# Performance work log

Hardware: AMD Instinct MI355X
Metric: run time of the kernel (lower is better)

Reference implementation:

```python
import jax, jax.numpy as jnp
import numpy as np

GROUPS = 8   # channels // group_size with group_size=8 for C=64
EPS = 1e-5


def group_norm_qc(x0, x1, gamma, beta):
    """LatticeGroupNorm: stats computed jointly over both cosets per (batch, group)."""
    B, C, H, W = x0.shape
    g = GROUPS
    xg = jnp.concatenate([x0.reshape(B, g, -1), x1.reshape(B, g, -1)], axis=-1)
    mean = xg.mean(axis=-1).reshape(B, g, 1, 1, 1)
    var = xg.var(axis=-1).reshape(B, g, 1, 1, 1)
    inv = jax.lax.rsqrt(var + EPS)
    ga = gamma[None, :, None, None]
    be = beta[None, :, None, None]

    def norm(x):
        xr = x.reshape(B, g, C // g, H, W)
        return ((xr - mean) * inv).reshape(B, C, H, W) * ga + be

    return norm(x0), norm(x1)


def qc_conv(x0, x1, w_center, w_corner, bias):
    """Quincunx LatticePad+LatticeConvolution with stencil
    [(0,0),(2,0),(0,2),(2,2),(1,1)], center (1,1).
    w_center: [O,I] tap (1,1) (same-coset 1x1).
    w_corner: [O,I,2,2] taps (0,0),(2,0),(0,2),(2,2) (cross-coset 2x2).
    Pad keeps output cosets the same size as inputs ('same' lattice conv)."""
    dn = ('NCHW', 'OIHW', 'NCHW')

    def c1(x):
        return jnp.einsum('oi,bihw->bohw', w_center, x)

    def c2(x, pad):
        return jax.lax.conv_general_dilated(x, w_corner, (1, 1), pad,
                                            dimension_numbers=dn)

    b = bias[None, :, None, None]
    # coset0 output gathers coset1 at (i-1+a, j-1+b) -> pad top/left
    out0 = c1(x0) + c2(x1, ((1, 0), (1, 0))) + b
    # coset1 output gathers coset0 at (i+a, j+b) -> pad bottom/right
    out1 = c1(x1) + c2(x0, ((0, 1), (0, 1))) + b
    return out0, out1


def setup_inputs() -> dict:
    key = jax.random.key(0)
    ks = jax.random.split(key, 10)
    B, C, H, W = 2, 64, 256, 256
    s = 0.05
    return {
        'x0': jax.random.normal(ks[0], (B, C, H, W), jnp.float32),
        'x1': jax.random.normal(ks[1], (B, C, H, W), jnp.float32),
        'g1': jnp.ones((C,), jnp.float32),
        'b1': jnp.zeros((C,), jnp.float32),
        'w1_center': jax.random.normal(ks[2], (C, C), jnp.float32) * s,
        'w1_corner': jax.random.normal(ks[3], (C, C, 2, 2), jnp.float32) * s,
        'bias1': jax.random.normal(ks[4], (C,), jnp.float32) * s,
        'g2': jnp.ones((C,), jnp.float32),
        'b2': jnp.zeros((C,), jnp.float32),
        'w2_center': jax.random.normal(ks[5], (C, C), jnp.float32) * s,
        'w2_corner': jax.random.normal(ks[6], (C, C, 2, 2), jnp.float32) * s,
        'bias2': jax.random.normal(ks[7], (C,), jnp.float32) * s,
        'w_skip': jax.random.normal(ks[8], (C, C), jnp.float32) * s,
        'bias_skip': jax.random.normal(ks[9], (C,), jnp.float32) * s,
        'g_skip': jnp.ones((C,), jnp.float32),
        'beta_skip': jnp.zeros((C,), jnp.float32),
    }


def reference(x0, x1, g1, b1, w1_center, w1_corner, bias1,
              g2, b2, w2_center, w2_corner, bias2,
              w_skip, bias_skip, g_skip, beta_skip):
    # conv path: GN -> ReLU -> pad+conv -> GN -> ReLU -> pad+conv
    h0, h1 = group_norm_qc(x0, x1, g1, b1)
    h0, h1 = jax.nn.relu(h0), jax.nn.relu(h1)
    h0, h1 = qc_conv(h0, h1, w1_center, w1_corner, bias1)
    h0, h1 = group_norm_qc(h0, h1, g2, b2)
    h0, h1 = jax.nn.relu(h0), jax.nn.relu(h1)
    h0, h1 = qc_conv(h0, h1, w2_center, w2_corner, bias2)
    # skip path: 1x1 lattice conv (stencil [(0,0)]) -> GN
    bsk = bias_skip[None, :, None, None]
    s0 = jnp.einsum('oi,bihw->bohw', w_skip, x0) + bsk
    s1 = jnp.einsum('oi,bihw->bohw', w_skip, x1) + bsk
    s0, s1 = group_norm_qc(s0, s1, g_skip, beta_skip)
    # residual add; stack the two cosets as leading axis for a single output
    return jnp.stack([h0 + s0, h1 + s1])
```

## Files before the change

kernel.cpp:

```cpp
#include <hip/hip_runtime.h>

typedef __attribute__((ext_vector_type(8))) __bf16 bf16x8;
typedef __attribute__((ext_vector_type(4))) __bf16 bf16x4;
typedef __attribute__((ext_vector_type(4))) float f32x4;

#define MFMA16(a,b,c) __builtin_amdgcn_mfma_f32_16x16x32_bf16(a,b,c,0,0,0)

static constexpr int HW = 65536;
static constexpr int WD = 256;
static constexpr int NB = 2;
static constexpr double INV_N = 1.0 / 1048576.0;
static constexpr float EPSV = 1e-5f;

static constexpr size_t OFF_P1  = 0;
static constexpr size_t OFF_P2  = 131072;
static constexpr size_t OFF_NRM = 196608;
static constexpr size_t OFF_A1  = 200704;
static constexpr size_t OFF_A2  = OFF_A1 + 40960;
static constexpr size_t OFF_XT  = OFF_A2 + 40960;
static constexpr size_t SZ_T    = (size_t)2 * NB * HW * 64 * 2;
static constexpr size_t OFF_S   = OFF_XT + SZ_T;
static constexpr size_t OFF_H   = OFF_S + SZ_T;

__global__ void k_prep(const float* __restrict__ wc1, const float* __restrict__ wk1,
                       const float* __restrict__ wc2, const float* __restrict__ wk2,
                       __bf16* __restrict__ A1, __bf16* __restrict__ A2) {
  const int stage = blockIdx.x;
  const float* wc = stage ? wc2 : wc1;
  const float* wk = stage ? wk2 : wk1;
  __bf16* A = stage ? A2 : A1;
  for (int idx = threadIdx.x; idx < 64 * 320; idx += blockDim.x) {
    int o = idx / 320, k = idx - o * 320;
    float v;
    if (k < 64) v = wc[o * 64 + k];
    else {
      int t = (k - 64) >> 6;
      int c = k & 63;
      v = wk[(o * 64 + c) * 4 + t];
    }
    A[idx] = (__bf16)v;
  }
}

__global__ __launch_bounds__(256) void k1(
    const float* __restrict__ x0, const float* __restrict__ x1,
    const float* __restrict__ wskip, const float* __restrict__ bskip,
    __bf16* __restrict__ xt, __bf16* __restrict__ sout, float* __restrict__ p1) {
  const int row = blockIdx.x;
  const int b   = blockIdx.y;
  const int co  = blockIdx.z;
  const float* x = co ? x1 : x0;
  __shared__ __attribute__((aligned(16))) __bf16 tile[256 * 72];
  __shared__ float redp[256];
  __shared__ float reds[32];
  const int t = threadIdx.x;
  const int wv = t >> 6, lane = t & 63;

  const float* xbase = x + (size_t)b * 64 * HW + (size_t)row * WD + t;
  __bf16* xtbase = xt + (((size_t)(co * NB + b) * HW) + (size_t)row * WD + t) * 64;

  float gsum[8], gsq[8];
#pragma unroll
  for (int g = 0; g < 8; ++g) { gsum[g] = 0.f; gsq[g] = 0.f; }
#pragma unroll
  for (int cg = 0; cg < 8; ++cg) {
    float f[8];
#pragma unroll
    for (int j = 0; j < 8; ++j) f[j] = xbase[(size_t)(cg * 8 + j) * HW];
    bf16x8 v;
#pragma unroll
    for (int j = 0; j < 8; ++j) {
      v[j] = (__bf16)f[j];
      gsum[cg] += f[j];
      gsq[cg] = fmaf(f[j], f[j], gsq[cg]);
    }
    *(bf16x8*)&tile[t * 72 + cg * 8] = v;
    *(bf16x8*)&xtbase[cg * 8] = v;
  }
#pragma unroll
  for (int g = 0; g < 8; ++g) {
#pragma unroll
    for (int m = 1; m < 16; m <<= 1) {
      gsum[g] += __shfl_xor(gsum[g], m, 64);
      gsq[g]  += __shfl_xor(gsq[g], m, 64);
    }
  }
  {
    const int q0 = lane >> 4;
    if ((lane & 15) == 0) {
#pragma unroll
      for (int g = 0; g < 8; ++g) {
        redp[(wv * 4 + q0) * 16 + g] = gsum[g];
        redp[(wv * 4 + q0) * 16 + 8 + g] = gsq[g];
      }
    }
  }
  __syncthreads();

  const int ln = lane & 15, q = lane >> 4;
  const int ch0 = wv * 16 + q * 4;
  bf16x8 a0, a1;
#pragma unroll
  for (int j = 0; j < 8; ++j) {
    a0[j] = (__bf16)wskip[(wv * 16 + ln) * 64 + q * 8 + j];
    a1[j] = (__bf16)wskip[(wv * 16 + ln) * 64 + 32 + q * 8 + j];
  }
  float bia[4];
#pragma unroll
  for (int r = 0; r < 4; ++r) bia[r] = bskip[ch0 + r];

  float ssum = 0.f, ssq = 0.f;
  for (int n = 0; n < 16; ++n) {
    f32x4 acc = {0.f, 0.f, 0.f, 0.f};
    bf16x8 b0 = *(const bf16x8*)&tile[(n * 16 + ln) * 72 + q * 8];
    bf16x8 b1 = *(const bf16x8*)&tile[(n * 16 + ln) * 72 + 32 + q * 8];
    acc = MFMA16(a0, b0, acc);
    acc = MFMA16(a1, b1, acc);
    bf16x4 sv;
    float v[4];
#pragma unroll
    for (int r = 0; r < 4; ++r) {
      v[r] = acc[r] + bia[r];
      ssum += v[r];
      ssq = fmaf(v[r], v[r], ssq);
      sv[r] = (__bf16)v[r];
    }
    size_t sb = ((size_t)(co * NB + b) * 4096 + row * 16 + n) * 1024 + (wv * 4 + q) * 64 + ln * 4;
    *(bf16x4*)&sout[sb] = sv;
  }
#pragma unroll
  for (int m = 1; m < 16; m <<= 1) {
    ssum += __shfl_xor(ssum, m, 64);
    ssq  += __shfl_xor(ssq, m, 64);
  }
  if ((lane & 15) == 0) {
    reds[wv * 4 + q] = ssum;
    reds[16 + wv * 4 + q] = ssq;
  }

  __syncthreads();
  if (t < 32) {
    float val;
    if (t < 16) {
      val = 0.f;
#pragma unroll
      for (int k = 0; k < 16; ++k) val += redp[k * 16 + t];
    } else {
      int kind = (t >> 3) & 1, g = t & 7;
      int wvv = g >> 1, qp = g & 1;
      val = reds[kind * 16 + wvv * 4 + qp * 2] + reds[kind * 16 + wvv * 4 + qp * 2 + 1];
    }
    const int bf1 = (co * 2 + b) * 256 + row;
    p1[(size_t)bf1 * 32 + t] = val;
  }
}

__global__ __launch_bounds__(256) void k_r1(
    const float* __restrict__ p1, const float* __restrict__ g1, const float* __restrict__ be1,
    const float* __restrict__ gsk, const float* __restrict__ besk, float* __restrict__ nrm) {
  const int t = threadIdx.x;
  __shared__ double red[64];
  const int sid = t >> 2, sub = t & 3;
  const int which = sid >> 5, b = (sid >> 4) & 1, kg = sid & 15;
  const int col = which * 16 + kg;
  double v = 0.0;
  for (int j = sub; j < 512; j += 4) {
    int co = j >> 8, rr = j & 255;
    v += (double)p1[((size_t)(co * 2 + b) * 256 + rr) * 32 + col];
  }
  v += __shfl_xor(v, 1, 64);
  v += __shfl_xor(v, 2, 64);
  if (sub == 0) red[sid] = v;
  __syncthreads();
  {
    int half = t >> 7;
    int b2 = (t >> 6) & 1, ch = t & 63, g = ch >> 3;
    int base = half * 32 + b2 * 16;
    double mean = red[base + g] * INV_N;
    double var  = red[base + 8 + g] * INV_N - mean * mean;
    float inv  = rsqrtf((float)var + EPSV);
    float ga = half ? gsk[ch] : g1[ch];
    float be = half ? besk[ch] : be1[ch];
    float sc = inv * ga;
    nrm[half * 256 + b2 * 128 + ch] = sc;
    nrm[half * 256 + b2 * 128 + 64 + ch] = be - (float)mean * sc;
  }
}

__global__ __launch_bounds__(256) void k2(
    const __bf16* __restrict__ xt, const __bf16* __restrict__ A1,
    const float* __restrict__ nrm, const float* __restrict__ bias1,
    __bf16* __restrict__ h, float* __restrict__ p2) {
  const int blk = ((blockIdx.x & 7) << 6) | (blockIdx.x >> 3);
  const int tx = blk & 15, ty = blk >> 4;
  const int b = blockIdx.y;
  const int y0p = ty * 8, x0p = tx * 16;
  __shared__ __attribute__((aligned(16))) __bf16 tl[2][153 * 72];
  __shared__ float sc[64], sh[64];
  __shared__ float lst[16];
  const int t = threadIdx.x;

  if (t < 64) {
    sc[t] = nrm[b * 128 + t];
    sh[t] = nrm[b * 128 + 64 + t];
  }
  if (t < 16) lst[t] = 0.f;
  __syncthreads();

#pragma unroll
  for (int i = 0; i < 10; ++i) {
    int u = t + i * 256;
    if (u < 2 * 153 * 8) {
      int cs = u / 1224;
      int rr = u - cs * 1224;
      int px = rr >> 3, cg = rr & 7;
      int ly = px / 17, lx = px - ly * 17;
      int gy = y0p + ly - cs, gx = x0p + lx - cs;
      bf16x8 v;
#pragma unroll
      for (int j = 0; j < 8; ++j) v[j] = (__bf16)0.f;
      if ((unsigned)gy < 256u && (unsigned)gx < 256u) {
        bf16x8 raw = *(const bf16x8*)&xt[(((size_t)(cs * NB + b) * WD + gy) * WD + gx) * 64 + cg * 8];
#pragma unroll
        for (int j = 0; j < 8; ++j) {
          float f = fmaf((float)raw[j], sc[cg * 8 + j], sh[cg * 8 + j]);
          v[j] = (__bf16)fmaxf(f, 0.f);
        }
      }
      *(bf16x8*)&tl[cs][px * 72 + cg * 8] = v;
    }
  }
  __syncthreads();

  const int wv = t >> 6, lane = t & 63, ln = lane & 15, q = lane >> 4;
  const int co = wv & 1, mh = wv >> 1;
  const int q8 = q * 8;
  bf16x8 af[2][10];
#pragma unroll
  for (int m = 0; m < 2; ++m)
#pragma unroll
    for (int kk = 0; kk < 10; ++kk)
      af[m][kk] = *(const bf16x8*)&A1[(mh * 32 + m * 16 + ln) * 320 + kk * 32 + q8];

  f32x4 acc[8][2];
#pragma unroll
  for (int n = 0; n < 8; ++n)
#pragma unroll
    for (int m = 0; m < 2; ++m) acc[n][m] = (f32x4){0.f, 0.f, 0.f, 0.f};

  const __bf16* tc = tl[co];
  const __bf16* to = tl[1 - co];
#pragma unroll
  for (int n = 0; n < 8; ++n) {
    const int cpix = co ? ((n + 1) * 17 + ln + 1) : (n * 17 + ln);
    const int tb = n * 17 + ln;
    const __bf16* pc = tc + cpix * 72 + q8;
    const __bf16* p0 = to + tb * 72 + q8;
    const __bf16* p1p = to + (tb + 1) * 72 + q8;
    const __bf16* p2p = to + (tb + 17) * 72 + q8;
    const __bf16* p3 = to + (tb + 18) * 72 + q8;
    bf16x8 bb;
    bb = *(const bf16x8*)pc;         acc[n][0]=MFMA16(af[0][0],bb,acc[n][0]); acc[n][1]=MFMA16(af[1][0],bb,acc[n][1]);
    bb = *(const bf16x8*)(pc + 32);  acc[n][0]=MFMA16(af[0][1],bb,acc[n][0]); acc[n][1]=MFMA16(af[1][1],bb,acc[n][1]);
    bb = *(const bf16x8*)p0;         acc[n][0]=MFMA16(af[0][2],bb,acc[n][0]); acc[n][1]=MFMA16(af[1][2],bb,acc[n][1]);
    bb = *(const bf16x8*)(p0 + 32);  acc[n][0]=MFMA16(af[0][3],bb,acc[n][0]); acc[n][1]=MFMA16(af[1][3],bb,acc[n][1]);
    bb = *(const bf16x8*)p1p;        acc[n][0]=MFMA16(af[0][4],bb,acc[n][0]); acc[n][1]=MFMA16(af[1][4],bb,acc[n][1]);
    bb = *(const bf16x8*)(p1p + 32); acc[n][0]=MFMA16(af[0][5],bb,acc[n][0]); acc[n][1]=MFMA16(af[1][5],bb,acc[n][1]);
    bb = *(const bf16x8*)p2p;        acc[n][0]=MFMA16(af[0][6],bb,acc[n][0]); acc[n][1]=MFMA16(af[1][6],bb,acc[n][1]);
    bb = *(const bf16x8*)(p2p + 32); acc[n][0]=MFMA16(af[0][7],bb,acc[n][0]); acc[n][1]=MFMA16(af[1][7],bb,acc[n][1]);
    bb = *(const bf16x8*)p3;         acc[n][0]=MFMA16(af[0][8],bb,acc[n][0]); acc[n][1]=MFMA16(af[1][8],bb,acc[n][1]);
    bb = *(const bf16x8*)(p3 + 32);  acc[n][0]=MFMA16(af[0][9],bb,acc[n][0]); acc[n][1]=MFMA16(af[1][9],bb,acc[n][1]);
  }

  __syncthreads();

  float s2s[2] = {0.f, 0.f}, s2q[2] = {0.f, 0.f};
  float bia[2][4];
#pragma unroll
  for (int m = 0; m < 2; ++m)
#pragma unroll
    for (int r = 0; r < 4; ++r) bia[m][r] = bias1[mh * 32 + m * 16 + q * 4 + r];

#pragma unroll
  for (int n = 0; n < 8; ++n)
#pragma unroll
    for (int m = 0; m < 2; ++m) {
      bf16x4 hv;
#pragma unroll
      for (int r = 0; r < 4; ++r) {
        float v = acc[n][m][r] + bia[m][r];
        s2s[m] += v;
        s2q[m] = fmaf(v, v, s2q[m]);
        hv[r] = (__bf16)v;
      }
      *(bf16x4*)&tl[co][(n * 16 + ln) * 72 + mh * 32 + m * 16 + q * 4] = hv;
    }

#pragma unroll
  for (int m = 0; m < 2; ++m) {
    float a_ = s2s[m], c_ = s2q[m];
#pragma unroll
    for (int mk = 1; mk < 32; mk <<= 1) {
      a_ += __shfl_xor(a_, mk, 64);
      c_ += __shfl_xor(c_, mk, 64);
    }
    if ((lane & 31) == 0) {
      int g = mh * 4 + m * 2 + (q >> 1);
      atomicAdd(&lst[g], a_);
      atomicAdd(&lst[8 + g], c_);
    }
  }
  __syncthreads();

#pragma unroll
  for (int i = 0; i < 8; ++i) {
    int co2 = i >> 2;
    int idx = (i & 3) * 256 + t;
    int px = idx >> 3, chunk = idx & 7;
    int gy = y0p + (px >> 4), gx = x0p + (px & 15);
    bf16x8 vv = *(const bf16x8*)&tl[co2][px * 72 + chunk * 8];
    *(bf16x8*)&h[(((size_t)(co2 * NB + b) * WD + gy) * WD + gx) * 64 + chunk * 8] = vv;
  }

  if (t < 16) p2[((size_t)b * 512 + blockIdx.x) * 16 + t] = lst[t];
}

__global__ __launch_bounds__(256) void k_r2(
    const float* __restrict__ p2, const float* __restrict__ g2, const float* __restrict__ be2,
    float* __restrict__ nrm) {
  const int t = threadIdx.x;
  __shared__ double red[32];
  const int sid = t >> 3, sub = t & 7;
  const int b = sid >> 4, col = sid & 15;
  double v = 0.0;
  for (int j = sub; j < 512; j += 8)
    v += (double)p2[((size_t)b * 512 + j) * 16 + col];
  v += __shfl_xor(v, 1, 64);
  v += __shfl_xor(v, 2, 64);
  v += __shfl_xor(v, 4, 64);
  if (sub == 0) red[sid] = v;
  __syncthreads();
  if (t < 128) {
    int b2 = t >> 6, ch = t & 63, g = ch >> 3;
    double mean = red[b2 * 16 + g] * INV_N;
    double var  = red[b2 * 16 + 8 + g] * INV_N - mean * mean;
    float inv  = rsqrtf((float)var + EPSV);
    float sc = inv * g2[ch];
    nrm[512 + b2 * 128 + ch] = sc;
    nrm[512 + b2 * 128 + 64 + ch] = be2[ch] - (float)mean * sc;
  }
}

__global__ __launch_bounds__(256) void k3(
    const __bf16* __restrict__ hin, const __bf16* __restrict__ A2,
    const float* __restrict__ nrm, const float* __restrict__ bias2,
    const __bf16* __restrict__ sin_, float* __restrict__ out) {
  const int blk = ((blockIdx.x & 7) << 6) | (blockIdx.x >> 3);
  const int tx = blk & 15, ty = blk >> 4;
  const int b = blockIdx.y;
  const int y0p = ty * 8, x0p = tx * 16;
  __shared__ __attribute__((aligned(16))) __bf16 tl[2][153 * 72];
  __shared__ float sc2[64], sh2[64], scS[64], shS[64];
  const int t = threadIdx.x;

  if (t < 64) {
    sc2[t] = nrm[512 + b * 128 + t];
    sh2[t] = nrm[512 + b * 128 + 64 + t];
    scS[t] = nrm[256 + b * 128 + t];
    shS[t] = nrm[256 + b * 128 + 64 + t];
  }
  __syncthreads();

#pragma unroll
  for (int i = 0; i < 10; ++i) {
    int u = t + i * 256;
    if (u < 2 * 153 * 8) {
      int cs = u / 1224;
      int rr = u - cs * 1224;
      int px = rr >> 3, cg = rr & 7;
      int ly = px / 17, lx = px - ly * 17;
      int gy = y0p + ly - cs, gx = x0p + lx - cs;
      bf16x8 v;
#pragma unroll
      for (int j = 0; j < 8; ++j) v[j] = (__bf16)0.f;
      if ((unsigned)gy < 256u && (unsigned)gx < 256u) {
        bf16x8 raw = *(const bf16x8*)&hin[(((size_t)(cs * NB + b) * WD + gy) * WD + gx) * 64 + cg * 8];
#pragma unroll
        for (int j = 0; j < 8; ++j) {
          float f = fmaf((float)raw[j], sc2[cg * 8 + j], sh2[cg * 8 + j]);
          v[j] = (__bf16)fmaxf(f, 0.f);
        }
      }
      *(bf16x8*)&tl[cs][px * 72 + cg * 8] = v;
    }
  }
  __syncthreads();

  const int wv = t >> 6, lane = t & 63, ln = lane & 15, q = lane >> 4;
  const int co = wv & 1, mh = wv >> 1;
  const int q8 = q * 8;
  bf16x8 af[2][10];
#pragma unroll
  for (int m = 0; m < 2; ++m)
#pragma unroll
    for (int kk = 0; kk < 10; ++kk)
      af[m][kk] = *(const bf16x8*)&A2[(mh * 32 + m * 16 + ln) * 320 + kk * 32 + q8];

  f32x4 acc[8][2];
#pragma unroll
  for (int n = 0; n < 8; ++n)
#pragma unroll
    for (int m = 0; m < 2; ++m) acc[n][m] = (f32x4){0.f, 0.f, 0.f, 0.f};

  const __bf16* tc = tl[co];
  const __bf16* to = tl[1 - co];
#pragma unroll
  for (int n = 0; n < 8; ++n) {
    const int cpix = co ? ((n + 1) * 17 + ln + 1) : (n * 17 + ln);
    const int tb = n * 17 + ln;
    const __bf16* pc = tc + cpix * 72 + q8;
    const __bf16* p0 = to + tb * 72 + q8;
    const __bf16* p1p = to + (tb + 1) * 72 + q8;
    const __bf16* p2p = to + (tb + 17) * 72 + q8;
    const __bf16* p3 = to + (tb + 18) * 72 + q8;
    bf16x8 bb;
    bb = *(const bf16x8*)pc;         acc[n][0]=MFMA16(af[0][0],bb,acc[n][0]); acc[n][1]=MFMA16(af[1][0],bb,acc[n][1]);
    bb = *(const bf16x8*)(pc + 32);  acc[n][0]=MFMA16(af[0][1],bb,acc[n][0]); acc[n][1]=MFMA16(af[1][1],bb,acc[n][1]);
    bb = *(const bf16x8*)p0;         acc[n][0]=MFMA16(af[0][2],bb,acc[n][0]); acc[n][1]=MFMA16(af[1][2],bb,acc[n][1]);
    bb = *(const bf16x8*)(p0 + 32);  acc[n][0]=MFMA16(af[0][3],bb,acc[n][0]); acc[n][1]=MFMA16(af[1][3],bb,acc[n][1]);
    bb = *(const bf16x8*)p1p;        acc[n][0]=MFMA16(af[0][4],bb,acc[n][0]); acc[n][1]=MFMA16(af[1][4],bb,acc[n][1]);
    bb = *(const bf16x8*)(p1p + 32); acc[n][0]=MFMA16(af[0][5],bb,acc[n][0]); acc[n][1]=MFMA16(af[1][5],bb,acc[n][1]);
    bb = *(const bf16x8*)p2p;        acc[n][0]=MFMA16(af[0][6],bb,acc[n][0]); acc[n][1]=MFMA16(af[1][6],bb,acc[n][1]);
    bb = *(const bf16x8*)(p2p + 32); acc[n][0]=MFMA16(af[0][7],bb,acc[n][0]); acc[n][1]=MFMA16(af[1][7],bb,acc[n][1]);
    bb = *(const bf16x8*)p3;         acc[n][0]=MFMA16(af[0][8],bb,acc[n][0]); acc[n][1]=MFMA16(af[1][8],bb,acc[n][1]);
    bb = *(const bf16x8*)(p3 + 32);  acc[n][0]=MFMA16(af[0][9],bb,acc[n][0]); acc[n][1]=MFMA16(af[1][9],bb,acc[n][1]);
  }

  float bia[2][4], sA[2][4], sB[2][4];
#pragma unroll
  for (int m = 0; m < 2; ++m)
#pragma unroll
    for (int r = 0; r < 4; ++r) {
      int ch = mh * 32 + m * 16 + q * 4 + r;
      bia[m][r] = bias2[ch];
      sA[m][r] = scS[ch];
      sB[m][r] = shS[ch];
    }

#pragma unroll
  for (int n = 0; n < 8; ++n) {
    int gy = y0p + n;
#pragma unroll
    for (int m = 0; m < 2; ++m) {
      int ch0 = mh * 32 + m * 16 + q * 4;
      size_t sb = ((size_t)(co * NB + b) * 4096 + gy * 16 + tx) * 1024 + (mh * 8 + m * 4 + q) * 64 + ln * 4;
      bf16x4 sv = *(const bf16x4*)&sin_[sb];
      size_t ob = ((size_t)(co * NB + b) * 64 + ch0) * HW + (size_t)gy * WD + x0p + ln;
#pragma unroll
      for (int r = 0; r < 4; ++r) {
        float v = acc[n][m][r] + bia[m][r] + fmaf((float)sv[r], sA[m][r], sB[m][r]);
        out[ob + (size_t)r * HW] = v;
      }
    }
  }
}

extern "C" void kernel_launch(void* const* d_in, const int* in_sizes, int n_in,
                              void* d_out, int out_size, void* d_ws, size_t ws_size,
                              hipStream_t stream) {
  (void)in_sizes; (void)n_in; (void)out_size; (void)ws_size;
  const float* x0    = (const float*)d_in[0];
  const float* x1    = (const float*)d_in[1];
  const float* g1    = (const float*)d_in[2];
  const float* b1    = (const float*)d_in[3];
  const float* w1c   = (const float*)d_in[4];
  const float* w1k   = (const float*)d_in[5];
  const float* bias1 = (const float*)d_in[6];
  const float* g2    = (const float*)d_in[7];
  const float* b2    = (const float*)d_in[8];
  const float* w2c   = (const float*)d_in[9];
  const float* w2k   = (const float*)d_in[10];
  const float* bias2 = (const float*)d_in[11];
  const float* wsk   = (const float*)d_in[12];
  const float* bsk   = (const float*)d_in[13];
  const float* gsk   = (const float*)d_in[14];
  const float* besk  = (const float*)d_in[15];

  char* ws = (char*)d_ws;
  float*  p1 = (float*)(ws + OFF_P1);
  float*  p2 = (float*)(ws + OFF_P2);
  float*  nrm = (float*)(ws + OFF_NRM);
  __bf16* A1 = (__bf16*)(ws + OFF_A1);
  __bf16* A2 = (__bf16*)(ws + OFF_A2);
  __bf16* xt = (__bf16*)(ws + OFF_XT);
  __bf16* s  = (__bf16*)(ws + OFF_S);
  __bf16* h  = (__bf16*)(ws + OFF_H);

  k_prep<<<2, 256, 0, stream>>>(w1c, w1k, w2c, w2k, A1, A2);
  k1<<<dim3(256, 2, 2), 256, 0, stream>>>(x0, x1, wsk, bsk, xt, s, p1);
  k_r1<<<1, 256, 0, stream>>>(p1, g1, b1, gsk, besk, nrm);
  k2<<<dim3(512, 2), 256, 0, stream>>>(xt, A1, nrm, bias1, h, p2);
  k_r2<<<1, 256, 0, stream>>>(p2, g2, b2, nrm);
  k3<<<dim3(512, 2), 256, 0, stream>>>(h, A2, nrm, bias2, s, (float*)d_out);
}
```

Measured before the change: 309.1 us.

## Fold weight prep and group-norm stat reductions into main kernels

Merges the weight-packing kernel into K1 as two extra blocks and removes the two single-block reduction kernels. Each block of K2 and K3 now reduces the per-row and per-tile partial sums itself to get the group-norm scale and shift. This cuts the pipeline from six launches to three and removes the serial single-block stages between them. The cost is that every block repeats the reduction, reading about 512 partials per column, which adds global traffic and latency at the start of each block.

```diff
diff --git a/kernel.cpp b/kernel.cpp
--- a/kernel.cpp
+++ b/kernel.cpp
@@ -14,7 +14,6 @@
 
 static constexpr size_t OFF_P1  = 0;
 static constexpr size_t OFF_P2  = 131072;
-static constexpr size_t OFF_NRM = 196608;
 static constexpr size_t OFF_A1  = 200704;
 static constexpr size_t OFF_A2  = OFF_A1 + 40960;
 static constexpr size_t OFF_XT  = OFF_A2 + 40960;
@@ -22,38 +21,42 @@
 static constexpr size_t OFF_S   = OFF_XT + SZ_T;
 static constexpr size_t OFF_H   = OFF_S + SZ_T;
 
-__global__ void k_prep(const float* __restrict__ wc1, const float* __restrict__ wk1,
-                       const float* __restrict__ wc2, const float* __restrict__ wk2,
-                       __bf16* __restrict__ A1, __bf16* __restrict__ A2) {
-  const int stage = blockIdx.x;
-  const float* wc = stage ? wc2 : wc1;
-  const float* wk = stage ? wk2 : wk1;
-  __bf16* A = stage ? A2 : A1;
-  for (int idx = threadIdx.x; idx < 64 * 320; idx += blockDim.x) {
-    int o = idx / 320, k = idx - o * 320;
-    float v;
-    if (k < 64) v = wc[o * 64 + k];
-    else {
-      int t = (k - 64) >> 6;
-      int c = k & 63;
-      v = wk[(o * 64 + c) * 4 + t];
-    }
-    A[idx] = (__bf16)v;
-  }
-}
-
-__global__ __launch_bounds__(256) void k1(
+__global__ __launch_bounds__(256) void K1(
     const float* __restrict__ x0, const float* __restrict__ x1,
     const float* __restrict__ wskip, const float* __restrict__ bskip,
-    __bf16* __restrict__ xt, __bf16* __restrict__ sout, float* __restrict__ p1) {
-  const int row = blockIdx.x;
-  const int b   = blockIdx.y;
-  const int co  = blockIdx.z;
+    const float* __restrict__ wc1, const float* __restrict__ wk1,
+    const float* __restrict__ wc2, const float* __restrict__ wk2,
+    __bf16* __restrict__ xt, __bf16* __restrict__ sout,
+    __bf16* __restrict__ A1, __bf16* __restrict__ A2, float* __restrict__ p1) {
+  const int bx = blockIdx.x;
+  const int t = threadIdx.x;
+
+  if (bx >= 1024) {
+    const int stage = bx - 1024;
+    const float* wc = stage ? wc2 : wc1;
+    const float* wk = stage ? wk2 : wk1;
+    __bf16* A = stage ? A2 : A1;
+    for (int idx = t; idx < 64 * 320; idx += 256) {
+      int o = idx / 320, k = idx - o * 320;
+      float v;
+      if (k < 64) v = wc[o * 64 + k];
+      else {
+        int tp = (k - 64) >> 6;
+        int c = k & 63;
+        v = wk[(o * 64 + c) * 4 + tp];
+      }
+      A[idx] = (__bf16)v;
+    }
+    return;
+  }
+
+  const int row = bx & 255;
+  const int b   = (bx >> 8) & 1;
+  const int co  = bx >> 9;
   const float* x = co ? x1 : x0;
   __shared__ __attribute__((aligned(16))) __bf16 tile[256 * 72];
   __shared__ float redp[256];
   __shared__ float reds[32];
-  const int t = threadIdx.x;
   const int wv = t >> 6, lane = t & 63;
 
   const float* xbase = x + (size_t)b * 64 * HW + (size_t)row * WD + t;
@@ -155,56 +158,45 @@
   }
 }
 
-__global__ __launch_bounds__(256) void k_r1(
+__global__ __launch_bounds__(256) void K2(
+    const __bf16* __restrict__ xt, const __bf16* __restrict__ A1,
     const float* __restrict__ p1, const float* __restrict__ g1, const float* __restrict__ be1,
-    const float* __restrict__ gsk, const float* __restrict__ besk, float* __restrict__ nrm) {
-  const int t = threadIdx.x;
-  __shared__ double red[64];
-  const int sid = t >> 2, sub = t & 3;
-  const int which = sid >> 5, b = (sid >> 4) & 1, kg = sid & 15;
-  const int col = which * 16 + kg;
-  double v = 0.0;
-  for (int j = sub; j < 512; j += 4) {
-    int co = j >> 8, rr = j & 255;
-    v += (double)p1[((size_t)(co * 2 + b) * 256 + rr) * 32 + col];
-  }
-  v += __shfl_xor(v, 1, 64);
-  v += __shfl_xor(v, 2, 64);
-  if (sub == 0) red[sid] = v;
-  __syncthreads();
-  {
-    int half = t >> 7;
-    int b2 = (t >> 6) & 1, ch = t & 63, g = ch >> 3;
-    int base = half * 32 + b2 * 16;
-    double mean = red[base + g] * INV_N;
-    double var  = red[base + 8 + g] * INV_N - mean * mean;
-    float inv  = rsqrtf((float)var + EPSV);
-    float ga = half ? gsk[ch] : g1[ch];
-    float be = half ? besk[ch] : be1[ch];
-    float sc = inv * ga;
-    nrm[half * 256 + b2 * 128 + ch] = sc;
-    nrm[half * 256 + b2 * 128 + 64 + ch] = be - (float)mean * sc;
-  }
-}
-
-__global__ __launch_bounds__(256) void k2(
-    const __bf16* __restrict__ xt, const __bf16* __restrict__ A1,
-    const float* __restrict__ nrm, const float* __restrict__ bias1,
+    const float* __restrict__ bias1,
     __bf16* __restrict__ h, float* __restrict__ p2) {
   const int blk = ((blockIdx.x & 7) << 6) | (blockIdx.x >> 3);
   const int tx = blk & 15, ty = blk >> 4;
   const int b = blockIdx.y;
   const int y0p = ty * 8, x0p = tx * 16;
   __shared__ __attribute__((aligned(16))) __bf16 tl[2][153 * 72];
+  __shared__ double redn[16];
   __shared__ float sc[64], sh[64];
   __shared__ float lst[16];
   const int t = threadIdx.x;
 
+  {
+    const int col = t >> 4, sub = t & 15;
+    double v = 0.0;
+    for (int j = sub; j < 512; j += 16) {
+      int cc = j >> 8, rr = j & 255;
+      v += (double)p1[((size_t)(cc * 2 + b) * 256 + rr) * 32 + col];
+    }
+    v += __shfl_xor(v, 1, 64);
+    v += __shfl_xor(v, 2, 64);
+    v += __shfl_xor(v, 4, 64);
+    v += __shfl_xor(v, 8, 64);
+    if (sub == 0) redn[col] = v;
+  }
+  if (t < 16) lst[t] = 0.f;
+  __syncthreads();
   if (t < 64) {
-    sc[t] = nrm[b * 128 + t];
-    sh[t] = nrm[b * 128 + 64 + t];
-  }
-  if (t < 16) lst[t] = 0.f;
+    int g = t >> 3;
+    double mean = redn[g] * INV_N;
+    double var  = redn[8 + g] * INV_N - mean * mean;
+    float inv = rsqrtf((float)var + EPSV);
+    float s_ = inv * g1[t];
+    sc[t] = s_;
+    sh[t] = be1[t] - (float)mean * s_;
+  }
   __syncthreads();
 
 #pragma unroll
@@ -325,49 +317,56 @@
   if (t < 16) p2[((size_t)b * 512 + blockIdx.x) * 16 + t] = lst[t];
 }
 
-__global__ __launch_bounds__(256) void k_r2(
-    const float* __restrict__ p2, const float* __restrict__ g2, const float* __restrict__ be2,
-    float* __restrict__ nrm) {
-  const int t = threadIdx.x;
-  __shared__ double red[32];
-  const int sid = t >> 3, sub = t & 7;
-  const int b = sid >> 4, col = sid & 15;
-  double v = 0.0;
-  for (int j = sub; j < 512; j += 8)
-    v += (double)p2[((size_t)b * 512 + j) * 16 + col];
-  v += __shfl_xor(v, 1, 64);
-  v += __shfl_xor(v, 2, 64);
-  v += __shfl_xor(v, 4, 64);
-  if (sub == 0) red[sid] = v;
-  __syncthreads();
-  if (t < 128) {
-    int b2 = t >> 6, ch = t & 63, g = ch >> 3;
-    double mean = red[b2 * 16 + g] * INV_N;
-    double var  = red[b2 * 16 + 8 + g] * INV_N - mean * mean;
-    float inv  = rsqrtf((float)var + EPSV);
-    float sc = inv * g2[ch];
-    nrm[512 + b2 * 128 + ch] = sc;
-    nrm[512 + b2 * 128 + 64 + ch] = be2[ch] - (float)mean * sc;
-  }
-}
-
-__global__ __launch_bounds__(256) void k3(
+__global__ __launch_bounds__(256) void K3(
     const __bf16* __restrict__ hin, const __bf16* __restrict__ A2,
-    const float* __restrict__ nrm, const float* __restrict__ bias2,
+    const float* __restrict__ p2, const float* __restrict__ p1,
+    const float* __restrict__ g2, const float* __restrict__ be2, const float* __restrict__ bias2,
+    const float* __restrict__ gsk, const float* __restrict__ besk,
     const __bf16* __restrict__ sin_, float* __restrict__ out) {
   const int blk = ((blockIdx.x & 7) << 6) | (blockIdx.x >> 3);
   const int tx = blk & 15, ty = blk >> 4;
   const int b = blockIdx.y;
   const int y0p = ty * 8, x0p = tx * 16;
   __shared__ __attribute__((aligned(16))) __bf16 tl[2][153 * 72];
+  __shared__ double redn[32];
   __shared__ float sc2[64], sh2[64], scS[64], shS[64];
   const int t = threadIdx.x;
 
-  if (t < 64) {
-    sc2[t] = nrm[512 + b * 128 + t];
-    sh2[t] = nrm[512 + b * 128 + 64 + t];
-    scS[t] = nrm[256 + b * 128 + t];
-    shS[t] = nrm[256 + b * 128 + 64 + t];
+  {
+    const int col = t >> 3, sub = t & 7;
+    double v = 0.0;
+    if (col < 16) {
+      for (int j = sub; j < 512; j += 8)
+        v += (double)p2[((size_t)b * 512 + j) * 16 + col];
+    } else {
+      for (int j = sub; j < 512; j += 8) {
+        int cc = j >> 8, rr = j & 255;
+        v += (double)p1[((size_t)(cc * 2 + b) * 256 + rr) * 32 + col];
+      }
+    }
+    v += __shfl_xor(v, 1, 64);
+    v += __shfl_xor(v, 2, 64);
+    v += __shfl_xor(v, 4, 64);
+    if (sub == 0) redn[col] = v;
+  }
+  __syncthreads();
+  if (t < 128) {
+    int half = t >> 6, ch = t & 63, g = ch >> 3;
+    if (half == 0) {
+      double mean = redn[g] * INV_N;
+      double var  = redn[8 + g] * INV_N - mean * mean;
+      float inv = rsqrtf((float)var + EPSV);
+      float s_ = inv * g2[ch];
+      sc2[ch] = s_;
+      sh2[ch] = be2[ch] - (float)mean * s_;
+    } else {
+      double mean = redn[16 + g] * INV_N;
+      double var  = redn[24 + g] * INV_N - mean * mean;
+      float inv = rsqrtf((float)var + EPSV);
+      float s_ = inv * gsk[ch];
+      scS[ch] = s_;
+      shS[ch] = besk[ch] - (float)mean * s_;
+    }
   }
   __syncthreads();
 
@@ -489,17 +488,13 @@
   char* ws = (char*)d_ws;
   float*  p1 = (float*)(ws + OFF_P1);
   float*  p2 = (float*)(ws + OFF_P2);
-  float*  nrm = (float*)(ws + OFF_NRM);
   __bf16* A1 = (__bf16*)(ws + OFF_A1);
   __bf16* A2 = (__bf16*)(ws + OFF_A2);
   __bf16* xt = (__bf16*)(ws + OFF_XT);
   __bf16* s  = (__bf16*)(ws + OFF_S);
   __bf16* h  = (__bf16*)(ws + OFF_H);
 
-  k_prep<<<2, 256, 0, stream>>>(w1c, w1k, w2c, w2k, A1, A2);
-  k1<<<dim3(256, 2, 2), 256, 0, stream>>>(x0, x1, wsk, bsk, xt, s, p1);
-  k_r1<<<1, 256, 0, stream>>>(p1, g1, b1, gsk, besk, nrm);
-  k2<<<dim3(512, 2), 256, 0, stream>>>(xt, A1, nrm, bias1, h, p2);
-  k_r2<<<1, 256, 0, stream>>>(p2, g2, b2, nrm);
-  k3<<<dim3(512, 2), 256, 0, stream>>>(h, A2, nrm, bias2, s, (float*)d_out);
+  K1<<<dim3(1026), 256, 0, stream>>>(x0, x1, wsk, bsk, w1c, w1k, w2c, w2k, xt, s, A1, A2, p1);
+  K2<<<dim3(512, 2), 256, 0, stream>>>(xt, A1, p1, g1, b1, bias1, h, p2);
+  K3<<<dim3(512, 2), 256, 0, stream>>>(h, A2, p2, p1, g2, b2, bias2, gsk, besk, s, (float*)d_out);
 }
```

Result: faster. 297.2 us (-3.9%).
